# Performance work log

Hardware: AMD Instinct MI355X
Metric: run time of the kernel (lower is better)

Reference implementation:

```python
import jax, jax.numpy as jnp
import numpy as np


def setup_inputs() -> dict:
    key = jax.random.key(0)
    ks = jax.random.split(key, 8)
    B, W, H, C = 4, 64, 64, 256
    C2 = C // 2
    s = 0.05
    x = jax.random.normal(ks[0], (B, W, H, C), dtype=jnp.float32)
    Wq = jax.random.normal(ks[1], (C, C2), dtype=jnp.float32) * s
    bq = jax.random.normal(ks[2], (C2,), dtype=jnp.float32) * s
    Wk = jax.random.normal(ks[3], (C, C2), dtype=jnp.float32) * s
    bk = jax.random.normal(ks[4], (C2,), dtype=jnp.float32) * s
    Wv = jax.random.normal(ks[5], (C, C), dtype=jnp.float32) * s
    bv = jax.random.normal(ks[6], (C,), dtype=jnp.float32) * s
    # gamma is initialized to 0 in the original; use a nonzero value so the
    # attention branch actually contributes (math is identical).
    gamma = jnp.array([0.5], dtype=jnp.float32)
    return {"x": x, "Wq": Wq, "bq": bq, "Wk": Wk, "bk": bk, "Wv": Wv, "bv": bv, "gamma": gamma}


def reference(x, Wq, bq, Wk, bk, Wv, bv, gamma):
    B, W, H, C = x.shape
    N = W * H
    # 1x1 convs == per-pixel linear projections
    q = jnp.einsum('bwhc,cd->bwhd', x, Wq) + bq   # [B,W,H,C/2]
    k = jnp.einsum('bwhc,cd->bwhd', x, Wk) + bk   # [B,W,H,C/2]
    v = jnp.einsum('bwhc,cd->bwhd', x, Wv) + bv   # [B,W,H,C]
    # Faithful to original: raw row-major reshape (B,W,H,Cq) -> (B,Cq,N)
    # (this mixes spatial and channel axes, exactly as the TF code does)
    pq = q.reshape(B, -1, N)                      # [B,C/2,N]
    pk = k.reshape(B, -1, N)                      # [B,C/2,N]
    pv = v.reshape(B, -1, N)                      # [B,C,N]
    energy = jnp.einsum('bcn,bcm->bnm', pq, pk)   # [B,N,N] (pq transposed)
    attention = jax.nn.softmax(energy, axis=-1)   # [B,N,N]
    out = jnp.einsum('bcm,bnm->bcn', pv, attention)  # pv @ attention^T
    out = out.reshape(B, W, H, C)
    return gamma * out + x
```

## Files before the change

### kernel.cpp

```cpp
#include <hip/hip_runtime.h>
#include <hip/hip_bf16.h>
#include <stdint.h>


typedef __attribute__((ext_vector_type(8)))  short short8;
typedef __attribute__((ext_vector_type(4)))  float f32x4;
typedef __attribute__((ext_vector_type(16))) float f32x16;
typedef __attribute__((ext_vector_type(4)))  unsigned short u16x4;

#define MFMA16 __builtin_amdgcn_mfma_f32_16x16x32_bf16
#define MFMA32 __builtin_amdgcn_mfma_f32_32x32x16_bf16

__device__ __forceinline__ unsigned short f2bf(float f) {
    union { float f; uint32_t u; } v; v.f = f;
    return (unsigned short)((v.u + 0x8000u) >> 16);
}
__device__ __forceinline__ float bf2f(unsigned short h) {
    union { uint32_t u; float f; } v; v.u = ((uint32_t)h) << 16;
    return v.f;
}
__device__ __forceinline__ uint32_t pkbf(float a, float b) {
    union { __hip_bfloat162 h; uint32_t u; } v;
    v.h = __float22bfloat162_rn(float2{a, b});
    return v.u;
}

__global__ void prep_w(const float* __restrict__ Wq, const float* __restrict__ bq,
                       const float* __restrict__ Wk, const float* __restrict__ bk,
                       const float* __restrict__ Wv, const float* __restrict__ bv,
                       unsigned short* __restrict__ Wt, float* __restrict__ bias) {
    int g = blockIdx.x * 256 + threadIdx.x;
    int c = g & 255, d = g >> 8;
    float val;
    if (d < 128)      val = Wq[c * 128 + d];
    else if (d < 256) val = Wk[c * 128 + (d - 128)];
    else              val = Wv[c * 256 + (d - 256)];
    Wt[d * 256 + c] = f2bf(val);
    if (g < 512) {
        float bb;
        if (g < 128)      bb = bq[g];
        else if (g < 256) bb = bk[g - 128];
        else              bb = bv[g - 256];
        bias[g] = bb;
    }
}

__global__ __launch_bounds__(256) void proj(
        const float* __restrict__ x, const unsigned short* __restrict__ Wt,
        const float* __restrict__ bias,
        unsigned short* __restrict__ Qrm, unsigned short* __restrict__ Kp,
        unsigned short* __restrict__ Vp) {
    __shared__ unsigned short T[128 * 136];
    int bid = blockIdx.x;
    int tid = threadIdx.x;
    int wave = tid >> 6, lane = tid & 63;
    int l16 = lane & 15, quad = lane >> 4;

    int kind, b, a, vh = 0;
    if (bid < 256) { kind = bid >> 7; int s = bid & 127; b = s >> 5; a = s & 31; }
    else           { kind = 2; int s = bid - 256; vh = s >> 7; b = (s >> 5) & 3; a = s & 31; }

    short8 af[2][8];
    #pragma unroll
    for (int g = 0; g < 2; ++g) {
        int p_local = wave * 32 + g * 16 + l16;
        int pix = (kind == 2) ? (b * 4096 + a * 128 + p_local)
                              : (b * 4096 + a + 32 * p_local);
        const float* xr = x + (size_t)pix * 256;
        #pragma unroll
        for (int kk = 0; kk < 8; ++kk) {
            f32x4 u0 = *(const f32x4*)(xr + kk * 32 + quad * 8);
            f32x4 u1 = *(const f32x4*)(xr + kk * 32 + quad * 8 + 4);
            union { short8 s; uint32_t u[4]; } h;
            h.u[0] = pkbf(u0[0], u0[1]); h.u[1] = pkbf(u0[2], u0[3]);
            h.u[2] = pkbf(u1[0], u1[1]); h.u[3] = pkbf(u1[2], u1[3]);
            af[g][kk] = h.s;
        }
    }

    if (kind < 2) {
        int dbase = kind * 128;
        #pragma unroll 1
        for (int dt = 0; dt < 8; ++dt) {
            int d = dbase + dt * 16 + l16;
            float bval = bias[d];
            f32x4 acc0 = {0.f,0.f,0.f,0.f}, acc1 = {0.f,0.f,0.f,0.f};
            #pragma unroll
            for (int kk = 0; kk < 8; ++kk) {
                short8 wrow = *(const short8*)(Wt + d * 256 + kk * 32 + quad * 8);
                acc0 = MFMA16(af[0][kk], wrow, acc0, 0, 0, 0);
                acc1 = MFMA16(af[1][kk], wrow, acc1, 0, 0, 0);
            }
            #pragma unroll
            for (int g = 0; g < 2; ++g) {
                f32x4 acc = g ? acc1 : acc0;
                union { u16x4 v; uint32_t u[2]; } pk;
                pk.u[0] = pkbf(acc[0] + bval, acc[1] + bval);
                pk.u[1] = pkbf(acc[2] + bval, acc[3] + bval);
                *(u16x4*)(T + (dt * 16 + l16) * 136 + wave * 32 + g * 16 + quad * 4) = pk.v;
            }
        }
        __syncthreads();
        if (kind == 0) {
            unsigned short* ob = Qrm + (b << 19) + a * 128 * 128;
            #pragma unroll
            for (int it = 0; it < 8; ++it) {
                int ci = it * 256 + tid;
                int row = ci >> 4, cj = ci & 15;
                *(short8*)(ob + row * 128 + cj * 8) = *(const short8*)(T + row * 136 + cj * 8);
            }
        } else {
            unsigned short* kb = Kp + (b << 19);
            #pragma unroll
            for (int it = 0; it < 8; ++it) {
                int ci = it * 256 + tid;
                int row = ci >> 4, cj = ci & 15;
                *(short8*)(kb + (cj >> 1) * 65536 + (a * 128 + row) * 16 + (cj & 1) * 8)
                    = *(const short8*)(T + row * 136 + cj * 8);
            }
        }
    } else {
        #pragma unroll 1
        for (int dt = 0; dt < 8; ++dt) {
            int d = 256 + vh * 128 + dt * 16 + l16;
            f32x4 acc0 = {0.f,0.f,0.f,0.f}, acc1 = {0.f,0.f,0.f,0.f};
            #pragma unroll
            for (int kk = 0; kk < 8; ++kk) {
                short8 wrow = *(const short8*)(Wt + d * 256 + kk * 32 + quad * 8);
                acc0 = MFMA16(wrow, af[0][kk], acc0, 0, 0, 0);
                acc1 = MFMA16(wrow, af[1][kk], acc1, 0, 0, 0);
            }
            int dvl = dt * 16 + quad * 4;
            f32x4 bv4 = *(const f32x4*)(bias + 256 + vh * 128 + dvl);
            #pragma unroll
            for (int g = 0; g < 2; ++g) {
                f32x4 acc = g ? acc1 : acc0;
                union { u16x4 v; uint32_t u[2]; } pk;
                pk.u[0] = pkbf(acc[0] + bv4[0], acc[1] + bv4[1]);
                pk.u[1] = pkbf(acc[2] + bv4[2], acc[3] + bv4[3]);
                int p_local = wave * 32 + g * 16 + l16;
                *(u16x4*)(T + p_local * 136 + dvl) = pk.v;
            }
        }
        __syncthreads();
        unsigned short* vb = Vp + (b << 20);
        #pragma unroll
        for (int it = 0; it < 8; ++it) {
            int cid = it * 256 + tid;
            int c_local = cid >> 8, w = cid & 255;
            int p_local = c_local * 16 + (w >> 4);
            int chunk = (w >> 4) * 16 + vh * 8 + ((w & 15) >> 1);
            *(short8*)(vb + chunk * 4096 + (a * 8 + c_local) * 16 + (w & 1) * 8)
                = *(const short8*)(T + p_local * 136 + (w & 15) * 8);
        }
    }
}

__global__ __launch_bounds__(256, 2) void attn(
        const unsigned short* __restrict__ Qrm, const unsigned short* __restrict__ Kp,
        const unsigned short* __restrict__ Vp, unsigned short* __restrict__ Opart,
        float* __restrict__ Lpart) {
    __shared__ unsigned short Ps[2 * 64 * 72];

    int bid = blockIdx.x;
    int comb = bid & 7, qt = bid >> 3;
    int b = comb >> 1, ks = comb & 1;
    int tid = threadIdx.x, wave = tid >> 6, lane = tid & 63;
    int l32 = lane & 31, half = lane >> 5;
    int mt = wave & 1, nt = wave >> 1;

    const unsigned short* Qb = Qrm + (b << 19);
    const unsigned short* Kb = Kp + (b << 19);
    const unsigned short* Vb = Vp + (b << 20);

    int q0 = qt * 64;

    short8 qf[8];
    {
        const unsigned short* qrow = Qb + (q0 + nt * 32 + l32) * 128 + half * 8;
        #pragma unroll
        for (int kk = 0; kk < 8; ++kk) qf[kk] = *(const short8*)(qrow + kk * 16);
    }

    f32x16 O[2][2];
    #pragma unroll
    for (int i = 0; i < 2; ++i)
        #pragma unroll
        for (int j = 0; j < 2; ++j)
            #pragma unroll
            for (int r = 0; r < 16; ++r) O[i][j][r] = 0.f;
    float l_run = 0.f;

    const int m_base = ks * 2048;
    const int chunk_base = ks * 128;
    const int kbase = (m_base + mt * 32 + l32) * 16 + half * 8;

    short8 kf[8];
    #pragma unroll
    for (int kk = 0; kk < 8; ++kk)
        kf[kk] = *(const short8*)(Kb + kk * 65536 + kbase);
    short8 vfrag[2][4];
    #pragma unroll
    for (int c2 = 0; c2 < 2; ++c2)
        #pragma unroll
        for (int k2 = 0; k2 < 4; ++k2)
            vfrag[c2][k2] = *(const short8*)(Vb + (chunk_base + k2) * 4096
                              + ((wave * 2 + c2) * 32 + l32) * 16 + half * 8);
    {
        f32x16 S;
        #pragma unroll
        for (int r = 0; r < 16; ++r) S[r] = 0.f;
        #pragma unroll
        for (int kk = 0; kk < 8; ++kk) S = MFMA32(kf[kk], qf[kk], S, 0, 0, 0);
        #pragma unroll
        for (int g = 0; g < 4; ++g) {
            float p0 = __expf(S[g * 4 + 0]), p1 = __expf(S[g * 4 + 1]);
            float p2 = __expf(S[g * 4 + 2]), p3 = __expf(S[g * 4 + 3]);
            l_run += (p0 + p1) + (p2 + p3);
            union { u16x4 v; uint32_t u[2]; } pk;
            pk.u[0] = pkbf(p0, p1); pk.u[1] = pkbf(p2, p3);
            *(u16x4*)(Ps + (nt * 32 + l32) * 72 + mt * 32 + g * 8 + half * 4) = pk.v;
        }
        #pragma unroll
        for (int kk = 0; kk < 8; ++kk)
            kf[kk] = *(const short8*)(Kb + kk * 65536 + 64 * 16 + kbase);
    }

    #pragma unroll 1
    for (int kt = 0; kt < 32; ++kt) {
        __syncthreads();

        if (kt < 31) {
            f32x16 S;
            #pragma unroll
            for (int r = 0; r < 16; ++r) S[r] = 0.f;
            #pragma unroll
            for (int kk = 0; kk < 8; ++kk) S = MFMA32(kf[kk], qf[kk], S, 0, 0, 0);
            if (kt < 30) {
                int kr = (kt + 2) * 64 * 16 + kbase;
                #pragma unroll
                for (int kk = 0; kk < 8; ++kk)
                    kf[kk] = *(const short8*)(Kb + kk * 65536 + kr);
            }
            unsigned short* Pn = Ps + ((kt + 1) & 1) * (64 * 72);
            #pragma unroll
            for (int g = 0; g < 4; ++g) {
                float p0 = __expf(S[g * 4 + 0]), p1 = __expf(S[g * 4 + 1]);
                float p2 = __expf(S[g * 4 + 2]), p3 = __expf(S[g * 4 + 3]);
                l_run += (p0 + p1) + (p2 + p3);
                union { u16x4 v; uint32_t u[2]; } pk;
                pk.u[0] = pkbf(p0, p1); pk.u[1] = pkbf(p2, p3);
                *(u16x4*)(Pn + (nt * 32 + l32) * 72 + mt * 32 + g * 8 + half * 4) = pk.v;
            }
        }

        unsigned short* Pb = Ps + (kt & 1) * (64 * 72);
        #pragma unroll
        for (int k2 = 0; k2 < 4; ++k2) {
            short8 pa0 = *(const short8*)(Pb + (l32) * 72 + k2 * 16 + half * 8);
            short8 pa1 = *(const short8*)(Pb + (32 + l32) * 72 + k2 * 16 + half * 8);
            O[0][0] = MFMA32(pa0, vfrag[0][k2], O[0][0], 0, 0, 0);
            O[0][1] = MFMA32(pa0, vfrag[1][k2], O[0][1], 0, 0, 0);
            O[1][0] = MFMA32(pa1, vfrag[0][k2], O[1][0], 0, 0, 0);
            O[1][1] = MFMA32(pa1, vfrag[1][k2], O[1][1], 0, 0, 0);
        }

        if (kt < 31) {
            int ch1 = chunk_base + (kt + 1) * 4;
            #pragma unroll
            for (int c2 = 0; c2 < 2; ++c2)
                #pragma unroll
                for (int k2 = 0; k2 < 4; ++k2)
                    vfrag[c2][k2] = *(const short8*)(Vb + (ch1 + k2) * 4096
                                      + ((wave * 2 + c2) * 32 + l32) * 16 + half * 8);
        }
    }

    l_run += __shfl_xor(l_run, 32);
    unsigned short* Op = Opart + ((size_t)(ks * 4 + b) << 20);
    #pragma unroll
    for (int q2 = 0; q2 < 2; ++q2)
        #pragma unroll
        for (int c2 = 0; c2 < 2; ++c2) {
            int c = (wave * 2 + c2) * 32 + l32;
            #pragma unroll
            for (int r = 0; r < 16; ++r) {
                int n = q0 + q2 * 32 + (r & 3) + 8 * (r >> 2) + 4 * half;
                Op[(size_t)n * 256 + c] = f2bf(O[q2][c2][r]);
            }
        }
    if (half == 0) {
        int n = q0 + nt * 32 + l32;
        Lpart[((ks * 2 + mt) * 4 + b) * 4096 + n] = l_run;
    }
}

__global__ __launch_bounds__(256) void merge_out(
        const unsigned short* __restrict__ Opart, const float* __restrict__ Lpart,
        const float* __restrict__ x, const float* __restrict__ gamma,
        float* __restrict__ out) {
    __shared__ float tile[64 * 257];
    __shared__ float wsm[64];
    int b  = blockIdx.x >> 6;
    int n0 = (blockIdx.x & 63) << 6;
    int tid = threadIdx.x;
    float g = gamma[0];
    if (tid < 64) {
        int n = n0 + tid;
        float L = 0.f;
        #pragma unroll
        for (int s = 0; s < 4; ++s) L += Lpart[(s * 4 + b) * 4096 + n];
        wsm[tid] = g / L;
    }
    __syncthreads();
    int nl1 = tid >> 5, cb1 = (tid & 31) * 8;
    const unsigned short* Op0 = Opart + ((size_t)b << 20);
    const unsigned short* Op1 = Opart + ((size_t)(4 + b) << 20);
    #pragma unroll
    for (int i = 0; i < 8; ++i) {
        int nl = i * 8 + nl1;
        size_t off = (size_t)(n0 + nl) * 256 + cb1;
        short8 o0 = *(const short8*)(Op0 + off);
        short8 o1 = *(const short8*)(Op1 + off);
        float w = wsm[nl];
        float* tr = tile + nl * 257 + cb1;
        #pragma unroll
        for (int e = 0; e < 8; ++e)
            tr[e] = (bf2f((unsigned short)o0[e]) + bf2f((unsigned short)o1[e])) * w;
    }
    __syncthreads();
    int cg = tid >> 4, nq = (tid & 15) * 4;
    #pragma unroll
    for (int it = 0; it < 16; ++it) {
        int c = it * 16 + cg;
        size_t idx = ((size_t)b << 20) + (size_t)c * 4096 + n0 + nq;
        f32x4 xv = *(const f32x4*)(x + idx);
        f32x4 ov;
        #pragma unroll
        for (int e = 0; e < 4; ++e) ov[e] = tile[(nq + e) * 257 + c] + xv[e];
        *(f32x4*)(out + idx) = ov;
    }
}

extern "C" void kernel_launch(void* const* d_in, const int* in_sizes, int n_in,
                              void* d_out, int out_size, void* d_ws, size_t ws_size,
                              hipStream_t stream) {
    const float* x     = (const float*)d_in[0];
    const float* Wq    = (const float*)d_in[1];
    const float* bq    = (const float*)d_in[2];
    const float* Wk    = (const float*)d_in[3];
    const float* bk    = (const float*)d_in[4];
    const float* Wv    = (const float*)d_in[5];
    const float* bv    = (const float*)d_in[6];
    const float* gamma = (const float*)d_in[7];
    float* out = (float*)d_out;

    if (ws_size < 34080768u) return;

    char* ws = (char*)d_ws;
    unsigned short* Wt    = (unsigned short*)(ws);
    float*          bias  = (float*)        (ws +   262144);
    unsigned short* Qrm   = (unsigned short*)(ws +   264192);
    unsigned short* Kp    = (unsigned short*)(ws +  4458496);
    unsigned short* Vp    = (unsigned short*)(ws +  8652800);
    unsigned short* Opart = (unsigned short*)(ws + 17041408);
    float*          Lpart = (float*)        (ws + 33818624);

    prep_w   <<<512, 256, 0, stream>>>(Wq, bq, Wk, bk, Wv, bv, Wt, bias);
    proj     <<<512, 256, 0, stream>>>(x, Wt, bias, Qrm, Kp, Vp);
    attn     <<<512, 256, 0, stream>>>(Qrm, Kp, Vp, Opart, Lpart);
    merge_out<<<256, 256, 0, stream>>>(Opart, Lpart, x, gamma, out);
}
```

Measured before the change: 170.9 us.

## Halve attention query tile to 32 rows, split S compute across wave pairs

The attention kernel now handles 32 query rows per block instead of 64 and launches twice as many blocks. Q is staged in shared memory, and the two wave pairs alternate computing S tiles for successive key blocks through a triple-buffered P array, while all four waves run the PV MFMAs. Row sums are reduced in LDS before they are written, so the merge kernel reads two partial sums instead of four. The goal is more blocks and higher occupancy (launch bounds 3), at the cost of K and V being re-read from global memory by twice as many blocks and lower MFMA reuse per block.

```diff
diff --git a/kernel.cpp b/kernel.cpp
--- a/kernel.cpp
+++ b/kernel.cpp
@@ -156,62 +156,78 @@
     }
 }
 
-__global__ __launch_bounds__(256, 2) void attn(
+__global__ __launch_bounds__(256, 3) void attn(
         const unsigned short* __restrict__ Qrm, const unsigned short* __restrict__ Kp,
         const unsigned short* __restrict__ Vp, unsigned short* __restrict__ Opart,
         float* __restrict__ Lpart) {
-    __shared__ unsigned short Ps[2 * 64 * 72];
+    __shared__ unsigned short Qs[32 * 136];
+    __shared__ unsigned short Ps[3 * 32 * 72];
+    __shared__ float Ls[128];
 
     int bid = blockIdx.x;
     int comb = bid & 7, qt = bid >> 3;
     int b = comb >> 1, ks = comb & 1;
     int tid = threadIdx.x, wave = tid >> 6, lane = tid & 63;
     int l32 = lane & 31, half = lane >> 5;
-    int mt = wave & 1, nt = wave >> 1;
+    int pair = wave >> 1, hp = wave & 1;
 
     const unsigned short* Qb = Qrm + (b << 19);
     const unsigned short* Kb = Kp + (b << 19);
     const unsigned short* Vb = Vp + (b << 20);
 
-    int q0 = qt * 64;
-
-    short8 qf[8];
+    int q0 = qt * 32;
+    const int kcol = half * 8;
+
     {
-        const unsigned short* qrow = Qb + (q0 + nt * 32 + l32) * 128 + half * 8;
-        #pragma unroll
-        for (int kk = 0; kk < 8; ++kk) qf[kk] = *(const short8*)(qrow + kk * 16);
-    }
-
-    f32x16 O[2][2];
-    #pragma unroll
-    for (int i = 0; i < 2; ++i)
-        #pragma unroll
-        for (int j = 0; j < 2; ++j)
-            #pragma unroll
-            for (int r = 0; r < 16; ++r) O[i][j][r] = 0.f;
+        int row = tid >> 3, col = (tid & 7) * 16;
+        const unsigned short* src = Qb + (q0 + row) * 128 + col;
+        *(short8*)(Qs + row * 136 + col)     = *(const short8*)(src);
+        *(short8*)(Qs + row * 136 + col + 8) = *(const short8*)(src + 8);
+    }
+
+    f32x16 O[2];
+    #pragma unroll
+    for (int j = 0; j < 2; ++j)
+        #pragma unroll
+        for (int r = 0; r < 16; ++r) O[j][r] = 0.f;
     float l_run = 0.f;
 
     const int m_base = ks * 2048;
-    const int chunk_base = ks * 128;
-    const int kbase = (m_base + mt * 32 + l32) * 16 + half * 8;
+    const int vchunk_base = ks * 128;
 
     short8 kf[8];
-    #pragma unroll
-    for (int kk = 0; kk < 8; ++kk)
-        kf[kk] = *(const short8*)(Kb + kk * 65536 + kbase);
+    {
+        int m = m_base + wave * 32 + l32;
+        #pragma unroll
+        for (int kk = 0; kk < 8; ++kk)
+            kf[kk] = *(const short8*)(Kb + kk * 65536 + m * 16 + kcol);
+    }
     short8 vfrag[2][4];
     #pragma unroll
     for (int c2 = 0; c2 < 2; ++c2)
         #pragma unroll
         for (int k2 = 0; k2 < 4; ++k2)
-            vfrag[c2][k2] = *(const short8*)(Vb + (chunk_base + k2) * 4096
-                              + ((wave * 2 + c2) * 32 + l32) * 16 + half * 8);
+            vfrag[c2][k2] = *(const short8*)(Vb + (vchunk_base + k2) * 4096
+                              + ((wave * 2 + c2) * 32 + l32) * 16 + kcol);
+
+    __syncthreads();
+
     {
         f32x16 S;
         #pragma unroll
         for (int r = 0; r < 16; ++r) S[r] = 0.f;
         #pragma unroll
-        for (int kk = 0; kk < 8; ++kk) S = MFMA32(kf[kk], qf[kk], S, 0, 0, 0);
+        for (int kk = 0; kk < 8; ++kk) {
+            short8 qf = *(const short8*)(Qs + l32 * 136 + kk * 16 + kcol);
+            S = MFMA32(kf[kk], qf, S, 0, 0, 0);
+        }
+        {
+            int m = m_base + (pair + 2) * 64 + hp * 32 + l32;
+            #pragma unroll
+            for (int kk = 0; kk < 8; ++kk)
+                kf[kk] = *(const short8*)(Kb + kk * 65536 + m * 16 + kcol);
+        }
+        unsigned short* Pn = Ps + pair * (32 * 72);
         #pragma unroll
         for (int g = 0; g < 4; ++g) {
             float p0 = __expf(S[g * 4 + 0]), p1 = __expf(S[g * 4 + 1]);
@@ -219,30 +235,43 @@
             l_run += (p0 + p1) + (p2 + p3);
             union { u16x4 v; uint32_t u[2]; } pk;
             pk.u[0] = pkbf(p0, p1); pk.u[1] = pkbf(p2, p3);
-            *(u16x4*)(Ps + (nt * 32 + l32) * 72 + mt * 32 + g * 8 + half * 4) = pk.v;
-        }
-        #pragma unroll
-        for (int kk = 0; kk < 8; ++kk)
-            kf[kk] = *(const short8*)(Kb + kk * 65536 + 64 * 16 + kbase);
+            *(u16x4*)(Pn + l32 * 72 + hp * 32 + g * 8 + half * 4) = pk.v;
+        }
     }
 
     #pragma unroll 1
-    for (int kt = 0; kt < 32; ++kt) {
+    for (int t = 0; t < 32; ++t) {
         __syncthreads();
 
-        if (kt < 31) {
-            f32x16 S;
+        bool active = (pair == (t & 1)) && (t < 30);
+
+        f32x16 S;
+        if (active) {
             #pragma unroll
             for (int r = 0; r < 16; ++r) S[r] = 0.f;
             #pragma unroll
-            for (int kk = 0; kk < 8; ++kk) S = MFMA32(kf[kk], qf[kk], S, 0, 0, 0);
-            if (kt < 30) {
-                int kr = (kt + 2) * 64 * 16 + kbase;
+            for (int kk = 0; kk < 8; ++kk) {
+                short8 qf = *(const short8*)(Qs + l32 * 136 + kk * 16 + kcol);
+                S = MFMA32(kf[kk], qf, S, 0, 0, 0);
+            }
+        }
+
+        const unsigned short* Pb = Ps + (t % 3) * (32 * 72);
+        #pragma unroll
+        for (int k2 = 0; k2 < 4; ++k2) {
+            short8 pa = *(const short8*)(Pb + l32 * 72 + k2 * 16 + kcol);
+            O[0] = MFMA32(pa, vfrag[0][k2], O[0], 0, 0, 0);
+            O[1] = MFMA32(pa, vfrag[1][k2], O[1], 0, 0, 0);
+        }
+
+        if (active) {
+            if (t < 28) {
+                int m = m_base + (t + 4) * 64 + hp * 32 + l32;
                 #pragma unroll
                 for (int kk = 0; kk < 8; ++kk)
-                    kf[kk] = *(const short8*)(Kb + kk * 65536 + kr);
-            }
-            unsigned short* Pn = Ps + ((kt + 1) & 1) * (64 * 72);
+                    kf[kk] = *(const short8*)(Kb + kk * 65536 + m * 16 + kcol);
+            }
+            unsigned short* Pn = Ps + ((t + 2) % 3) * (32 * 72);
             #pragma unroll
             for (int g = 0; g < 4; ++g) {
                 float p0 = __expf(S[g * 4 + 0]), p1 = __expf(S[g * 4 + 1]);
@@ -250,48 +279,37 @@
                 l_run += (p0 + p1) + (p2 + p3);
                 union { u16x4 v; uint32_t u[2]; } pk;
                 pk.u[0] = pkbf(p0, p1); pk.u[1] = pkbf(p2, p3);
-                *(u16x4*)(Pn + (nt * 32 + l32) * 72 + mt * 32 + g * 8 + half * 4) = pk.v;
-            }
-        }
-
-        unsigned short* Pb = Ps + (kt & 1) * (64 * 72);
-        #pragma unroll
-        for (int k2 = 0; k2 < 4; ++k2) {
-            short8 pa0 = *(const short8*)(Pb + (l32) * 72 + k2 * 16 + half * 8);
-            short8 pa1 = *(const short8*)(Pb + (32 + l32) * 72 + k2 * 16 + half * 8);
-            O[0][0] = MFMA32(pa0, vfrag[0][k2], O[0][0], 0, 0, 0);
-            O[0][1] = MFMA32(pa0, vfrag[1][k2], O[0][1], 0, 0, 0);
-            O[1][0] = MFMA32(pa1, vfrag[0][k2], O[1][0], 0, 0, 0);
-            O[1][1] = MFMA32(pa1, vfrag[1][k2], O[1][1], 0, 0, 0);
-        }
-
-        if (kt < 31) {
-            int ch1 = chunk_base + (kt + 1) * 4;
+                *(u16x4*)(Pn + l32 * 72 + hp * 32 + g * 8 + half * 4) = pk.v;
+            }
+        }
+
+        if (t < 31) {
+            int ch = vchunk_base + (t + 1) * 4;
             #pragma unroll
             for (int c2 = 0; c2 < 2; ++c2)
                 #pragma unroll
                 for (int k2 = 0; k2 < 4; ++k2)
-                    vfrag[c2][k2] = *(const short8*)(Vb + (ch1 + k2) * 4096
-                                      + ((wave * 2 + c2) * 32 + l32) * 16 + half * 8);
+                    vfrag[c2][k2] = *(const short8*)(Vb + (ch + k2) * 4096
+                                      + ((wave * 2 + c2) * 32 + l32) * 16 + kcol);
         }
     }
 
     l_run += __shfl_xor(l_run, 32);
     unsigned short* Op = Opart + ((size_t)(ks * 4 + b) << 20);
     #pragma unroll
-    for (int q2 = 0; q2 < 2; ++q2)
-        #pragma unroll
-        for (int c2 = 0; c2 < 2; ++c2) {
-            int c = (wave * 2 + c2) * 32 + l32;
-            #pragma unroll
-            for (int r = 0; r < 16; ++r) {
-                int n = q0 + q2 * 32 + (r & 3) + 8 * (r >> 2) + 4 * half;
-                Op[(size_t)n * 256 + c] = f2bf(O[q2][c2][r]);
-            }
-        }
-    if (half == 0) {
-        int n = q0 + nt * 32 + l32;
-        Lpart[((ks * 2 + mt) * 4 + b) * 4096 + n] = l_run;
+    for (int c2 = 0; c2 < 2; ++c2) {
+        int c = (wave * 2 + c2) * 32 + l32;
+        #pragma unroll
+        for (int r = 0; r < 16; ++r) {
+            int n = q0 + (r & 3) + 8 * (r >> 2) + 4 * half;
+            Op[(size_t)n * 256 + c] = f2bf(O[c2][r]);
+        }
+    }
+    if (lane < 32) Ls[wave * 32 + lane] = l_run;
+    __syncthreads();
+    if (tid < 32) {
+        float L = (Ls[tid] + Ls[32 + tid]) + (Ls[64 + tid] + Ls[96 + tid]);
+        Lpart[((size_t)(ks * 4 + b)) * 4096 + q0 + tid] = L;
     }
 }
 
@@ -309,7 +327,7 @@
         int n = n0 + tid;
         float L = 0.f;
         #pragma unroll
-        for (int s = 0; s < 4; ++s) L += Lpart[(s * 4 + b) * 4096 + n];
+        for (int s = 0; s < 2; ++s) L += Lpart[(s * 4 + b) * 4096 + n];
         wsm[tid] = g / L;
     }
     __syncthreads();
@@ -368,6 +386,6 @@
 
     prep_w   <<<512, 256, 0, stream>>>(Wq, bq, Wk, bk, Wv, bv, Wt, bias);
     proj     <<<512, 256, 0, stream>>>(x, Wt, bias, Qrm, Kp, Vp);
-    attn     <<<512, 256, 0, stream>>>(Qrm, Kp, Vp, Opart, Lpart);
+    attn     <<<1024, 256, 0, stream>>>(Qrm, Kp, Vp, Opart, Lpart);
     merge_out<<<256, 256, 0, stream>>>(Opart, Lpart, x, gamma, out);
 }
```

After: 187.3 us. +9.6%, slower.

## Split attention keys four ways and reduce partials with fp32 atomics

Applied to the files above, without the earlier changes.

The attention kernel now splits the key dimension into four slices instead of two, doubling the grid to 1024 blocks and raising the occupancy hint to three blocks per CU. Partial outputs and row sums are accumulated with fp32 atomicAdd into a single zeroed buffer instead of being written as separate bf16 partials, which simplifies the merge kernel to one fp32 read per element. The aim is better CU utilisation and shorter per-block loops, at the cost of two memsets, many global atomics and more fp32 traffic.

```diff
diff --git a/kernel.cpp b/kernel.cpp
--- a/kernel.cpp
+++ b/kernel.cpp
@@ -156,15 +156,16 @@
     }
 }
 
-__global__ __launch_bounds__(256, 2) void attn(
+__global__ __launch_bounds__(256, 3) void attn(
         const unsigned short* __restrict__ Qrm, const unsigned short* __restrict__ Kp,
-        const unsigned short* __restrict__ Vp, unsigned short* __restrict__ Opart,
+        const unsigned short* __restrict__ Vp, float* __restrict__ Opart,
         float* __restrict__ Lpart) {
     __shared__ unsigned short Ps[2 * 64 * 72];
+    __shared__ float Ls[128];
 
     int bid = blockIdx.x;
-    int comb = bid & 7, qt = bid >> 3;
-    int b = comb >> 1, ks = comb & 1;
+    int comb = bid & 15, qt = bid >> 4;
+    int b = comb >> 2, ks = comb & 3;
     int tid = threadIdx.x, wave = tid >> 6, lane = tid & 63;
     int l32 = lane & 31, half = lane >> 5;
     int mt = wave & 1, nt = wave >> 1;
@@ -191,8 +192,8 @@
             for (int r = 0; r < 16; ++r) O[i][j][r] = 0.f;
     float l_run = 0.f;
 
-    const int m_base = ks * 2048;
-    const int chunk_base = ks * 128;
+    const int m_base = ks * 1024;
+    const int chunk_base = ks * 64;
     const int kbase = (m_base + mt * 32 + l32) * 16 + half * 8;
 
     short8 kf[8];
@@ -227,16 +228,16 @@
     }
 
     #pragma unroll 1
-    for (int kt = 0; kt < 32; ++kt) {
+    for (int kt = 0; kt < 16; ++kt) {
         __syncthreads();
 
-        if (kt < 31) {
+        if (kt < 15) {
             f32x16 S;
             #pragma unroll
             for (int r = 0; r < 16; ++r) S[r] = 0.f;
             #pragma unroll
             for (int kk = 0; kk < 8; ++kk) S = MFMA32(kf[kk], qf[kk], S, 0, 0, 0);
-            if (kt < 30) {
+            if (kt < 14) {
                 int kr = (kt + 2) * 64 * 16 + kbase;
                 #pragma unroll
                 for (int kk = 0; kk < 8; ++kk)
@@ -265,7 +266,7 @@
             O[1][1] = MFMA32(pa1, vfrag[1][k2], O[1][1], 0, 0, 0);
         }
 
-        if (kt < 31) {
+        if (kt < 15) {
             int ch1 = chunk_base + (kt + 1) * 4;
             #pragma unroll
             for (int c2 = 0; c2 < 2; ++c2)
@@ -277,7 +278,7 @@
     }
 
     l_run += __shfl_xor(l_run, 32);
-    unsigned short* Op = Opart + ((size_t)(ks * 4 + b) << 20);
+    float* Op = Opart + ((size_t)b << 20);
     #pragma unroll
     for (int q2 = 0; q2 < 2; ++q2)
         #pragma unroll
@@ -286,17 +287,20 @@
             #pragma unroll
             for (int r = 0; r < 16; ++r) {
                 int n = q0 + q2 * 32 + (r & 3) + 8 * (r >> 2) + 4 * half;
-                Op[(size_t)n * 256 + c] = f2bf(O[q2][c2][r]);
-            }
-        }
-    if (half == 0) {
-        int n = q0 + nt * 32 + l32;
-        Lpart[((ks * 2 + mt) * 4 + b) * 4096 + n] = l_run;
+                atomicAdd(&Op[(size_t)n * 256 + c], O[q2][c2][r]);
+            }
+        }
+    if (half == 0) Ls[wave * 32 + l32] = l_run;
+    __syncthreads();
+    if (tid < 64) {
+        int nt_ = tid >> 5, l = tid & 31;
+        float L = Ls[(nt_ * 2) * 32 + l] + Ls[(nt_ * 2 + 1) * 32 + l];
+        atomicAdd(&Lpart[b * 4096 + q0 + nt_ * 32 + l], L);
     }
 }
 
 __global__ __launch_bounds__(256) void merge_out(
-        const unsigned short* __restrict__ Opart, const float* __restrict__ Lpart,
+        const float* __restrict__ Opart, const float* __restrict__ Lpart,
         const float* __restrict__ x, const float* __restrict__ gamma,
         float* __restrict__ out) {
     __shared__ float tile[64 * 257];
@@ -305,28 +309,22 @@
     int n0 = (blockIdx.x & 63) << 6;
     int tid = threadIdx.x;
     float g = gamma[0];
-    if (tid < 64) {
-        int n = n0 + tid;
-        float L = 0.f;
-        #pragma unroll
-        for (int s = 0; s < 4; ++s) L += Lpart[(s * 4 + b) * 4096 + n];
-        wsm[tid] = g / L;
-    }
+    if (tid < 64) wsm[tid] = g / Lpart[b * 4096 + n0 + tid];
     __syncthreads();
     int nl1 = tid >> 5, cb1 = (tid & 31) * 8;
-    const unsigned short* Op0 = Opart + ((size_t)b << 20);
-    const unsigned short* Op1 = Opart + ((size_t)(4 + b) << 20);
+    const float* Op = Opart + ((size_t)b << 20);
     #pragma unroll
     for (int i = 0; i < 8; ++i) {
         int nl = i * 8 + nl1;
         size_t off = (size_t)(n0 + nl) * 256 + cb1;
-        short8 o0 = *(const short8*)(Op0 + off);
-        short8 o1 = *(const short8*)(Op1 + off);
+        f32x4 a0 = *(const f32x4*)(Op + off);
+        f32x4 a1 = *(const f32x4*)(Op + off + 4);
         float w = wsm[nl];
         float* tr = tile + nl * 257 + cb1;
         #pragma unroll
-        for (int e = 0; e < 8; ++e)
-            tr[e] = (bf2f((unsigned short)o0[e]) + bf2f((unsigned short)o1[e])) * w;
+        for (int e = 0; e < 4; ++e) tr[e]     = a0[e] * w;
+        #pragma unroll
+        for (int e = 0; e < 4; ++e) tr[4 + e] = a1[e] * w;
     }
     __syncthreads();
     int cg = tid >> 4, nq = (tid & 15) * 4;
@@ -363,11 +361,13 @@
     unsigned short* Qrm   = (unsigned short*)(ws +   264192);
     unsigned short* Kp    = (unsigned short*)(ws +  4458496);
     unsigned short* Vp    = (unsigned short*)(ws +  8652800);
-    unsigned short* Opart = (unsigned short*)(ws + 17041408);
+    float*          Opart = (float*)        (ws + 17041408);
     float*          Lpart = (float*)        (ws + 33818624);
 
+    hipMemsetAsync(Opart, 0, 16777216u, stream);
+    hipMemsetAsync(Lpart, 0, 65536u, stream);
     prep_w   <<<512, 256, 0, stream>>>(Wq, bq, Wk, bk, Wv, bv, Wt, bias);
     proj     <<<512, 256, 0, stream>>>(x, Wt, bias, Qrm, Kp, Vp);
-    attn     <<<512, 256, 0, stream>>>(Qrm, Kp, Vp, Opart, Lpart);
+    attn     <<<1024, 256, 0, stream>>>(Qrm, Kp, Vp, Opart, Lpart);
     merge_out<<<256, 256, 0, stream>>>(Opart, Lpart, x, gamma, out);
 }
```

New measurement: 240.1 us. 40.5% more time.

## Fuse Q/K projection blocks and software-pipeline QK scores one tile ahead

Applied to the files above, without the earlier changes.

The projection kernel now makes one block compute both the Q and K projections for the same pixel group. This reuses the converted x fragments and cuts the grid from 512 to 384 blocks, at the cost of longer per-block work. In the attention kernel, the QK^T score MFMA for tile kt+1 is computed one iteration earlier and held in a saved register set, and K fragments are prefetched three tiles ahead. The aim is to overlap the exp/softmax work with independent MFMAs, in exchange for higher register pressure.

```diff
diff --git a/kernel.cpp b/kernel.cpp
--- a/kernel.cpp
+++ b/kernel.cpp
@@ -57,8 +57,8 @@
     int l16 = lane & 15, quad = lane >> 4;
 
     int kind, b, a, vh = 0;
-    if (bid < 256) { kind = bid >> 7; int s = bid & 127; b = s >> 5; a = s & 31; }
-    else           { kind = 2; int s = bid - 256; vh = s >> 7; b = (s >> 5) & 3; a = s & 31; }
+    if (bid < 128) { kind = 0; b = bid >> 5; a = bid & 31; }
+    else           { kind = 2; int s = bid - 128; vh = s >> 7; b = (s >> 5) & 3; a = s & 31; }
 
     short8 af[2][8];
     #pragma unroll
@@ -78,45 +78,49 @@
         }
     }
 
-    if (kind < 2) {
-        int dbase = kind * 128;
+    if (kind == 0) {
         #pragma unroll 1
-        for (int dt = 0; dt < 8; ++dt) {
-            int d = dbase + dt * 16 + l16;
-            float bval = bias[d];
-            f32x4 acc0 = {0.f,0.f,0.f,0.f}, acc1 = {0.f,0.f,0.f,0.f};
-            #pragma unroll
-            for (int kk = 0; kk < 8; ++kk) {
-                short8 wrow = *(const short8*)(Wt + d * 256 + kk * 32 + quad * 8);
-                acc0 = MFMA16(af[0][kk], wrow, acc0, 0, 0, 0);
-                acc1 = MFMA16(af[1][kk], wrow, acc1, 0, 0, 0);
-            }
-            #pragma unroll
-            for (int g = 0; g < 2; ++g) {
-                f32x4 acc = g ? acc1 : acc0;
-                union { u16x4 v; uint32_t u[2]; } pk;
-                pk.u[0] = pkbf(acc[0] + bval, acc[1] + bval);
-                pk.u[1] = pkbf(acc[2] + bval, acc[3] + bval);
-                *(u16x4*)(T + (dt * 16 + l16) * 136 + wave * 32 + g * 16 + quad * 4) = pk.v;
-            }
-        }
-        __syncthreads();
-        if (kind == 0) {
-            unsigned short* ob = Qrm + (b << 19) + a * 128 * 128;
-            #pragma unroll
-            for (int it = 0; it < 8; ++it) {
-                int ci = it * 256 + tid;
-                int row = ci >> 4, cj = ci & 15;
-                *(short8*)(ob + row * 128 + cj * 8) = *(const short8*)(T + row * 136 + cj * 8);
-            }
-        } else {
-            unsigned short* kb = Kp + (b << 19);
-            #pragma unroll
-            for (int it = 0; it < 8; ++it) {
-                int ci = it * 256 + tid;
-                int row = ci >> 4, cj = ci & 15;
-                *(short8*)(kb + (cj >> 1) * 65536 + (a * 128 + row) * 16 + (cj & 1) * 8)
-                    = *(const short8*)(T + row * 136 + cj * 8);
+        for (int phase = 0; phase < 2; ++phase) {
+            int dbase = phase * 128;
+            #pragma unroll 1
+            for (int dt = 0; dt < 8; ++dt) {
+                int d = dbase + dt * 16 + l16;
+                float bval = bias[d];
+                f32x4 acc0 = {0.f,0.f,0.f,0.f}, acc1 = {0.f,0.f,0.f,0.f};
+                #pragma unroll
+                for (int kk = 0; kk < 8; ++kk) {
+                    short8 wrow = *(const short8*)(Wt + d * 256 + kk * 32 + quad * 8);
+                    acc0 = MFMA16(af[0][kk], wrow, acc0, 0, 0, 0);
+                    acc1 = MFMA16(af[1][kk], wrow, acc1, 0, 0, 0);
+                }
+                #pragma unroll
+                for (int g = 0; g < 2; ++g) {
+                    f32x4 acc = g ? acc1 : acc0;
+                    union { u16x4 v; uint32_t u[2]; } pk;
+                    pk.u[0] = pkbf(acc[0] + bval, acc[1] + bval);
+                    pk.u[1] = pkbf(acc[2] + bval, acc[3] + bval);
+                    *(u16x4*)(T + (dt * 16 + l16) * 136 + wave * 32 + g * 16 + quad * 4) = pk.v;
+                }
+            }
+            __syncthreads();
+            if (phase == 0) {
+                unsigned short* ob = Qrm + (b << 19) + a * 128 * 128;
+                #pragma unroll
+                for (int it = 0; it < 8; ++it) {
+                    int ci = it * 256 + tid;
+                    int row = ci >> 4, cj = ci & 15;
+                    *(short8*)(ob + row * 128 + cj * 8) = *(const short8*)(T + row * 136 + cj * 8);
+                }
+                __syncthreads();
+            } else {
+                unsigned short* kb = Kp + (b << 19);
+                #pragma unroll
+                for (int it = 0; it < 8; ++it) {
+                    int ci = it * 256 + tid;
+                    int row = ci >> 4, cj = ci & 15;
+                    *(short8*)(kb + (cj >> 1) * 65536 + (a * 128 + row) * 16 + (cj & 1) * 8)
+                        = *(const short8*)(T + row * 136 + cj * 8);
+                }
             }
         }
     } else {
@@ -221,9 +225,19 @@
             pk.u[0] = pkbf(p0, p1); pk.u[1] = pkbf(p2, p3);
             *(u16x4*)(Ps + (nt * 32 + l32) * 72 + mt * 32 + g * 8 + half * 4) = pk.v;
         }
+    }
+    f32x16 Ssave;
+    {
         #pragma unroll
         for (int kk = 0; kk < 8; ++kk)
             kf[kk] = *(const short8*)(Kb + kk * 65536 + 64 * 16 + kbase);
+        #pragma unroll
+        for (int r = 0; r < 16; ++r) Ssave[r] = 0.f;
+        #pragma unroll
+        for (int kk = 0; kk < 8; ++kk) Ssave = MFMA32(kf[kk], qf[kk], Ssave, 0, 0, 0);
+        #pragma unroll
+        for (int kk = 0; kk < 8; ++kk)
+            kf[kk] = *(const short8*)(Kb + kk * 65536 + 2 * 64 * 16 + kbase);
     }
 
     #pragma unroll 1
@@ -231,27 +245,30 @@
         __syncthreads();
 
         if (kt < 31) {
-            f32x16 S;
-            #pragma unroll
-            for (int r = 0; r < 16; ++r) S[r] = 0.f;
-            #pragma unroll
-            for (int kk = 0; kk < 8; ++kk) S = MFMA32(kf[kk], qf[kk], S, 0, 0, 0);
-            if (kt < 30) {
-                int kr = (kt + 2) * 64 * 16 + kbase;
-                #pragma unroll
-                for (int kk = 0; kk < 8; ++kk)
-                    kf[kk] = *(const short8*)(Kb + kk * 65536 + kr);
-            }
             unsigned short* Pn = Ps + ((kt + 1) & 1) * (64 * 72);
             #pragma unroll
             for (int g = 0; g < 4; ++g) {
-                float p0 = __expf(S[g * 4 + 0]), p1 = __expf(S[g * 4 + 1]);
-                float p2 = __expf(S[g * 4 + 2]), p3 = __expf(S[g * 4 + 3]);
+                float p0 = __expf(Ssave[g * 4 + 0]), p1 = __expf(Ssave[g * 4 + 1]);
+                float p2 = __expf(Ssave[g * 4 + 2]), p3 = __expf(Ssave[g * 4 + 3]);
                 l_run += (p0 + p1) + (p2 + p3);
                 union { u16x4 v; uint32_t u[2]; } pk;
                 pk.u[0] = pkbf(p0, p1); pk.u[1] = pkbf(p2, p3);
                 *(u16x4*)(Pn + (nt * 32 + l32) * 72 + mt * 32 + g * 8 + half * 4) = pk.v;
             }
+        }
+
+        f32x16 Snew;
+        if (kt < 30) {
+            #pragma unroll
+            for (int r = 0; r < 16; ++r) Snew[r] = 0.f;
+            #pragma unroll
+            for (int kk = 0; kk < 8; ++kk) Snew = MFMA32(kf[kk], qf[kk], Snew, 0, 0, 0);
+        }
+        if (kt < 29) {
+            int kr = (kt + 3) * 64 * 16 + kbase;
+            #pragma unroll
+            for (int kk = 0; kk < 8; ++kk)
+                kf[kk] = *(const short8*)(Kb + kk * 65536 + kr);
         }
 
         unsigned short* Pb = Ps + (kt & 1) * (64 * 72);
@@ -274,6 +291,8 @@
                     vfrag[c2][k2] = *(const short8*)(Vb + (ch1 + k2) * 4096
                                       + ((wave * 2 + c2) * 32 + l32) * 16 + half * 8);
         }
+
+        if (kt < 30) Ssave = Snew;
     }
 
     l_run += __shfl_xor(l_run, 32);
@@ -367,7 +386,7 @@
     float*          Lpart = (float*)        (ws + 33818624);
 
     prep_w   <<<512, 256, 0, stream>>>(Wq, bq, Wk, bk, Wv, bv, Wt, bias);
-    proj     <<<512, 256, 0, stream>>>(x, Wt, bias, Qrm, Kp, Vp);
+    proj     <<<384, 256, 0, stream>>>(x, Wt, bias, Qrm, Kp, Vp);
     attn     <<<512, 256, 0, stream>>>(Qrm, Kp, Vp, Opart, Lpart);
     merge_out<<<256, 256, 0, stream>>>(Opart, Lpart, x, gamma, out);
 }
```

Measured after the change: 183.9 us. 7.6% more time.
